# Kernel tuning notes

Hardware: AMD Instinct MI355X
Metric: run time of the kernel (lower is better)

The kernel has to match this reference:

```python
import jax, jax.numpy as jnp
import numpy as np

B, N, E, D = 2, 4096, 1024, 128  # batch, seq, embed_dim, expand_ratio (head dim)
H = E // D                        # 8 heads
LN_EPS = 1e-5


def setup_inputs() -> dict:
    key = jax.random.key(0)
    ks = jax.random.split(key, 6)
    s = 0.02
    return {
        "x": jax.random.normal(ks[0], (B, N, E), jnp.float32),
        "W_in": jax.random.normal(ks[1], (3 * E, E), jnp.float32) * s,
        "W_out": jax.random.normal(ks[2], (E, E), jnp.float32) * s,
        "W_g1": jax.random.normal(ks[3], (D, E), jnp.float32) * s,
        "W_g2": jax.random.normal(ks[4], (E, D), jnp.float32) * s,
        "ln_w": jnp.ones((E,), jnp.float32),
    }


def _gla_scan(q, k, v, g):
    # q,k,v,g: [b,h,n,d]; GLA recurrence: S_t = exp(g_t)[:,None]*S_{t-1} + k_t v_t^T; o_t = q_t @ S_t
    def step(S, inp):
        qt, kt, vt, gt = inp  # each [b,h,d]
        S = jnp.exp(gt)[..., None] * S + kt[..., None] * vt[..., None, :]  # [b,h,d,d]
        ot = jnp.einsum('bhd,bhde->bhe', qt, S)
        return S, ot

    xs = tuple(jnp.moveaxis(a, 2, 0) for a in (q, k, v, g))  # [n,b,h,d]
    S0 = jnp.zeros(q.shape[:2] + (q.shape[-1], v.shape[-1]), q.dtype)
    _, o = jax.lax.scan(step, S0, xs)
    return jnp.moveaxis(o, 0, 2)  # [b,h,n,d]


def reference(x, W_in, W_out, W_g1, W_g2, ln_w):
    b, n, e = x.shape
    u = x @ W_in.T                       # [b,n,3E]
    v, q, lg = jnp.split(u, 3, axis=-1)  # note order: v, q, log_f
    q = jax.nn.silu(q)                   # q_activation = silu
    f = jax.nn.sigmoid(lg)
    k = 1.0 - f                          # non_sparse_ratio == 1 path
    g = jax.nn.log_sigmoid(lg)           # log of forget gate

    def tohead(a):
        return a.reshape(b, n, H, D).transpose(0, 2, 1, 3)  # b h n d

    o = _gla_scan(tohead(q), tohead(k), tohead(v), tohead(g))
    o = o.transpose(0, 2, 1, 3).reshape(b, n, e)  # b n (h d)

    gate = jax.nn.sigmoid((x @ W_g1.T) @ W_g2.T)  # low-rank output gate
    o = o * gate

    mu = jnp.mean(o, axis=-1, keepdims=True)
    var = jnp.var(o, axis=-1, keepdims=True)
    o = (o - mu) * jax.lax.rsqrt(var + LN_EPS) * ln_w  # layernorm, no bias
    return o @ W_out.T
```

## Files before the change

### kernel.cpp

```cpp
#include <hip/hip_runtime.h>
#include <cmath>

#define B_ 2
#define N_ 4096
#define E_ 1024
#define D_ 128
#define H_ 8
#define CHUNK 64
#define NC_ (N_/CHUNK)

__device__ __forceinline__ float sigmoidf_(float x){ return 1.f/(1.f + __expf(-x)); }

__device__ __forceinline__ unsigned short f2bf(float f){
    unsigned u = __float_as_uint(f);
    u += 0x7FFFu + ((u >> 16) & 1u);
    return (unsigned short)(u >> 16);
}
__device__ __forceinline__ float bf2f(unsigned short s){
    return __uint_as_float(((unsigned)s) << 16);
}
__device__ __forceinline__ unsigned short f2bf_fast(float f){
    __bf16 h = (__bf16)f;
    return __builtin_bit_cast(unsigned short, h);
}

typedef __attribute__((ext_vector_type(8))) __bf16 bf16x8;
typedef __attribute__((ext_vector_type(4))) float  f32x4;
typedef __attribute__((address_space(3))) unsigned int as3_u32;
typedef __attribute__((address_space(1))) unsigned int as1_u32;

__device__ __forceinline__ void gload_lds16(const void* g, void* l){
    __builtin_amdgcn_global_load_lds((as1_u32*)g, (as3_u32*)l, 16, 0, 0);
}

__device__ __forceinline__ bf16x8 ldsfrag256(const unsigned short* Lp, int row, int kg){
    return *reinterpret_cast<const bf16x8*>(&Lp[row*128 + ((kg ^ (row&7))<<3)]);
}
__device__ __forceinline__ bf16x8 ldsfrag128(const unsigned short* Lp, int row, int kg){
    return *reinterpret_cast<const bf16x8*>(&Lp[row*64 + ((kg ^ (row&7))<<3)]);
}
__device__ __forceinline__ bf16x8 u4_to_bf(uint4 u){
    return __builtin_bit_cast(bf16x8, u);
}

template<bool OUT_BF16>
__global__ __launch_bounds__(256) void gemm_bf16(
    const unsigned short* __restrict__ A,
    const unsigned short* __restrict__ Bw,
    void* __restrict__ Cout, int M, int N, int K)
{
    __shared__ unsigned short As[128*64];
    __shared__ unsigned short Bs[128*64];
    const int tid  = threadIdx.x;
    const int wave = tid >> 6;
    const int lane = tid & 63;
    const int gx = gridDim.x;
    const int nwg = gx * gridDim.y;
    int bid = blockIdx.y*gx + blockIdx.x;
    bid = (bid & 7)*(nwg >> 3) + (bid >> 3);
    const int m0 = (bid / gx) * 128, n0 = (bid % gx) * 128;
    const int wr = (wave >> 1) * 64;
    const int wc = (wave & 1) * 64;
    const int l15 = lane & 15, l4 = lane >> 4;
    const int p = l15 & 7;

    f32x4 acc[4][4];
#pragma unroll
    for (int i=0;i<4;i++)
#pragma unroll
        for (int j=0;j<4;j++)
#pragma unroll
            for (int q=0;q<4;q++) acc[i][j][q]=0.f;

    const int srow = wave*32 + (lane>>3);
    const int sgrp = lane & 7;

    for (int k0=0; k0<K; k0+=64){
        if (k0) __syncthreads();
#pragma unroll
        for (int i=0;i<4;i++){
            const int r  = srow + 8*i;
            const int cg = sgrp ^ (r & 7);
            gload_lds16(A  + (size_t)(m0 + r)*K + k0 + cg*8, &As[(wave*32 + 8*i)*64]);
            gload_lds16(Bw + (size_t)(n0 + r)*K + k0 + cg*8, &Bs[(wave*32 + 8*i)*64]);
        }
        __syncthreads();
#pragma unroll
        for (int ks=0; ks<2; ks++){
            bf16x8 av[4], bv[4];
            const int tA = (((ks<<2) | l4) ^ p) << 3;
#pragma unroll
            for (int f=0; f<4; f++){
                const int rowA = wr + f*16 + l15;
                const int rowB = wc + f*16 + l15;
                av[f] = *reinterpret_cast<const bf16x8*>(&As[(rowA<<6) + tA]);
                bv[f] = *reinterpret_cast<const bf16x8*>(&Bs[(rowB<<6) + tA]);
            }
#pragma unroll
            for (int fm=0; fm<4; fm++)
#pragma unroll
                for (int fn=0; fn<4; fn++)
                    acc[fm][fn] = __builtin_amdgcn_mfma_f32_16x16x32_bf16(
                        av[fm], bv[fn], acc[fm][fn], 0, 0, 0);
        }
    }
    const int crow0 = m0 + wr + l4*4;
    const int ccol0 = n0 + wc + l15;
    if (!OUT_BF16){
        float* C = (float*)Cout;
#pragma unroll
        for (int fm=0; fm<4; fm++)
#pragma unroll
            for (int fn=0; fn<4; fn++)
#pragma unroll
                for (int j=0;j<4;j++)
                    C[(size_t)(crow0 + fm*16 + j)*N + ccol0 + fn*16] = acc[fm][fn][j];
    } else {
        unsigned short* C = (unsigned short*)Cout;
#pragma unroll
        for (int fm=0; fm<4; fm++)
#pragma unroll
            for (int fn=0; fn<4; fn++)
#pragma unroll
                for (int j=0;j<4;j++)
                    C[(size_t)(crow0 + fm*16 + j)*N + ccol0 + fn*16] = f2bf(acc[fm][fn][j]);
    }
}

#define CQ0 2097152
#define CQ1 786432
#define CQ2 262144
#define CQ3 32768
#define CQ4 32768
__global__ __launch_bounds__(256) void cast_all(
    const float* __restrict__ x,  const float* __restrict__ w1,
    const float* __restrict__ w2, const float* __restrict__ w3,
    const float* __restrict__ w4,
    unsigned short* __restrict__ xb,  unsigned short* __restrict__ w1b,
    unsigned short* __restrict__ w2b, unsigned short* __restrict__ w3b,
    unsigned short* __restrict__ w4b)
{
    const int total = CQ0+CQ1+CQ2+CQ3+CQ4;
    for (int i = blockIdx.x*256 + threadIdx.x; i < total; i += gridDim.x*256){
        const float* src; unsigned short* dst; int off;
        if (i < CQ0){ src=x; dst=xb; off=i; }
        else if (i < CQ0+CQ1){ src=w1; dst=w1b; off=i-CQ0; }
        else if (i < CQ0+CQ1+CQ2){ src=w2; dst=w2b; off=i-CQ0-CQ1; }
        else if (i < CQ0+CQ1+CQ2+CQ3){ src=w3; dst=w3b; off=i-CQ0-CQ1-CQ2; }
        else { src=w4; dst=w4b; off=i-CQ0-CQ1-CQ2-CQ3; }
        const float4 v = reinterpret_cast<const float4*>(src)[off];
        ushort4 o;
        o.x = f2bf(v.x); o.y = f2bf(v.y); o.z = f2bf(v.z); o.w = f2bf(v.w);
        reinterpret_cast<ushort4*>(dst)[off] = o;
    }
}

__global__ __launch_bounds__(512) void gla_prep(
    const unsigned short* __restrict__ u, float* __restrict__ EBC,
    unsigned short* __restrict__ QSb, unsigned short* __restrict__ KINb,
    unsigned short* __restrict__ KINtb, unsigned short* __restrict__ Vtb)
{
    __shared__ float tot[4*128];
    const int bid = blockIdx.x;
    const int c  = bid % NC_;
    const int hh = (bid / NC_) % H_;
    const int b  = bid / (NC_*H_);
    const int d  = threadIdx.x & 127;
    const int qd = threadIdx.x >> 7;
    const int t0 = qd*16;
    const size_t urow0 = ((size_t)b*N_ + (size_t)c*CHUNK)*(3*E_) + (size_t)hh*D_ + d;

    float bl[16], qv[16], vv[16];
#pragma unroll
    for (int i=0;i<16;i++)
        bl[i] = bf2f(u[urow0 + (size_t)(t0+i)*(3*E_) + 2*E_]);
#pragma unroll
    for (int i=0;i<16;i++)
        qv[i] = bf2f(u[urow0 + (size_t)(t0+i)*(3*E_) + E_]);
#pragma unroll
    for (int i=0;i<16;i++)
        vv[i] = bf2f(u[urow0 + (size_t)(t0+i)*(3*E_)]);

    float acc = 0.f;
#pragma unroll
    for (int i=0;i<16;i++){
        const float lg = bl[i];
        const float e  = __expf(-fabsf(lg));
        const float g  = fminf(lg, 0.f) - __logf(1.f + e);
        acc += g;
        bl[i] = acc;
    }
    tot[qd*128 + d] = acc;
    __syncthreads();
    const float s0 = tot[d], s1 = tot[128+d], s2 = tot[256+d], s3 = tot[384+d];
    const float off = (qd>0 ? s0 : 0.f) + (qd>1 ? s1 : 0.f) + (qd>2 ? s2 : 0.f);
    const float bcv = s0 + s1 + s2 + s3;
    const float ebc = __expf(bcv);
    if (threadIdx.x < 128) EBC[(size_t)bid*D_ + d] = ebc;

    unsigned kin_pk[8], v_pk[8];
    float prev = 0.f;
    const size_t obase = (size_t)bid*CHUNK*D_;
#pragma unroll
    for (int i=0;i<16;i++){
        const int t = t0 + i;
        const float Bl = bl[i];
        const float g  = Bl - prev;  prev = Bl;
        const float Bc = Bl + off;
        const float kk = 1.f - __expf(g);
        const float eB = __expf(Bc);
        const float q  = qv[i];
        const float es = __expf(-q);
        const float silu = q * __builtin_amdgcn_rcpf(1.f + es);
        const float qs  = silu * eB;
        const float kin = kk * __builtin_amdgcn_rcpf(eB);
        QSb [obase + (size_t)t*D_ + d] = f2bf_fast(qs);
        KINb[obase + (size_t)t*D_ + d] = f2bf_fast(kin);
        const unsigned kb = f2bf_fast(kin * ebc);
        const unsigned vb = f2bf_fast(vv[i]);
        if (i & 1){ kin_pk[i>>1] |= kb<<16; v_pk[i>>1] |= vb<<16; }
        else      { kin_pk[i>>1]  = kb;     v_pk[i>>1]  = vb;     }
    }
    const size_t tbase = (size_t)bid*D_*CHUNK + (size_t)d*CHUNK + t0;
#pragma unroll
    for (int j=0;j<2;j++){
        uint4 kq, vq;
        kq.x=kin_pk[4*j]; kq.y=kin_pk[4*j+1]; kq.z=kin_pk[4*j+2]; kq.w=kin_pk[4*j+3];
        vq.x=v_pk[4*j];   vq.y=v_pk[4*j+1];   vq.z=v_pk[4*j+2];   vq.w=v_pk[4*j+3];
        *reinterpret_cast<uint4*>(&KINtb[tbase + j*8]) = kq;
        *reinterpret_cast<uint4*>(&Vtb  [tbase + j*8]) = vq;
    }
}

__global__ __launch_bounds__(256) void gla_chunk_mm(
    const unsigned short* __restrict__ Vtb,
    const unsigned short* __restrict__ KINtb,
    unsigned short* __restrict__ McTb)
{
    __shared__ unsigned short As[128*64];
    __shared__ unsigned short Bs[128*64];
    const int bid = blockIdx.x;
    const int tid = threadIdx.x;
    const int w = tid >> 6, lane = tid & 63;
    const int l15 = lane & 15, l4 = lane >> 4;
    const int wr = (w >> 1) * 64, wc = (w & 1) * 64;
    const unsigned short* A  = Vtb   + (size_t)bid*128*64;
    const unsigned short* Bp = KINtb + (size_t)bid*128*64;

    f32x4 acc[4][4];
#pragma unroll
    for (int i=0;i<4;i++)
#pragma unroll
        for (int j=0;j<4;j++)
#pragma unroll
            for (int q=0;q<4;q++) acc[i][j][q]=0.f;

#pragma unroll
    for (int i=0;i<4;i++){
        const int r  = w*32 + i*8 + (lane>>3);
        const int gs = (lane&7) ^ (r&7);
        gload_lds16(A  + (size_t)r*64 + gs*8, &As[(w*32+i*8)*64]);
        gload_lds16(Bp + (size_t)r*64 + gs*8, &Bs[(w*32+i*8)*64]);
    }
    __syncthreads();
#pragma unroll
    for (int ks=0; ks<2; ks++){
        bf16x8 av[4], bv[4];
#pragma unroll
        for (int f=0; f<4; f++){
            av[f] = ldsfrag128(As, wr + f*16 + l15, ks*4 + l4);
            bv[f] = ldsfrag128(Bs, wc + f*16 + l15, ks*4 + l4);
        }
#pragma unroll
        for (int fm=0; fm<4; fm++)
#pragma unroll
            for (int fn=0; fn<4; fn++)
                acc[fm][fn] = __builtin_amdgcn_mfma_f32_16x16x32_bf16(
                    av[fm], bv[fn], acc[fm][fn], 0, 0, 0);
    }
    unsigned short* C = McTb + (size_t)bid*128*128;
#pragma unroll
    for (int fm=0; fm<4; fm++)
#pragma unroll
        for (int fn=0; fn<4; fn++)
#pragma unroll
            for (int j=0;j<4;j++)
                C[(size_t)(wr + fm*16 + l4*4 + j)*128 + wc + fn*16 + l15] = f2bf(acc[fm][fn][j]);
}

__global__ __launch_bounds__(256) void gla_scan_chunks(
    const unsigned short* __restrict__ McTb, const float* __restrict__ EBC,
    unsigned short* __restrict__ Sb16)
{
    const size_t F = (size_t)blockIdx.x*256 + threadIdx.x;
    const int bh = (int)(F >> 14);
    const int rem = (int)(F & 16383);
    const int d = rem & 127;
    float S = 0.f;
    for (int c=0;c<NC_;c++){
        const size_t idx = (((size_t)bh*NC_ + c) << 14) + rem;
        const float m = bf2f(McTb[idx]);
        const float dec = EBC[((size_t)bh*NC_ + c)*D_ + d];
        Sb16[idx] = f2bf(S);
        S = dec*S + m;
    }
}

__global__ __launch_bounds__(256) void gla_output(
    const unsigned short* __restrict__ QSb,
    const unsigned short* __restrict__ KINb,
    const unsigned short* __restrict__ Vtb,
    const unsigned short* __restrict__ Sb,
    const unsigned short* __restrict__ G2b,
    unsigned short* __restrict__ Opre)
{
    __shared__ unsigned short QS_l[64*128];
    __shared__ unsigned short A_l [64*64];
    const int bid = blockIdx.x;
    const int c = bid % NC_;
    const int h = (bid / NC_) % H_;
    const int b = bid / (NC_*H_);
    const int tid = threadIdx.x;
    const int w = tid >> 6, lane = tid & 63;
    const int l15 = lane & 15, l4 = lane >> 4;

    const unsigned short* qb = QSb + (size_t)bid*64*128;
    const unsigned short* kb = KINb + (size_t)bid*64*128;
    const unsigned short* vb = Vtb + (size_t)bid*128*64;
    const unsigned short* sb = Sb  + (size_t)bid*128*128;

#pragma unroll
    for (int i=0;i<4;i++){
        const int r  = w*16 + i*4 + (lane>>4);
        const int gs = (lane&15) ^ (r&7);
        gload_lds16(qb + (size_t)r*128 + gs*8, &QS_l[(w*16+i*4)*128]);
    }
    uint4 kinr[4];
    {
        const int srow = w*16 + l15;
#pragma unroll
        for (int ks=0; ks<4; ks++)
            kinr[ks] = *reinterpret_cast<const uint4*>(kb + (size_t)srow*128 + (ks*4 + l4)*8);
    }
    __syncthreads();

    uint4 vtr[2][2], sr[2][4];
#pragma unroll
    for (int fe=0; fe<2; fe++){
        const int row = w*32 + fe*16 + l15;
#pragma unroll
        for (int ks=0; ks<2; ks++)
            vtr[fe][ks] = *reinterpret_cast<const uint4*>(vb + (size_t)row*64 + (ks*4 + l4)*8);
#pragma unroll
        for (int ks=0; ks<4; ks++)
            sr[fe][ks]  = *reinterpret_cast<const uint4*>(sb + (size_t)row*128 + (ks*4 + l4)*8);
    }

    f32x4 accA[4];
#pragma unroll
    for (int i=0;i<4;i++)
#pragma unroll
        for (int q=0;q<4;q++) accA[i][q]=0.f;
#pragma unroll
    for (int ks=0; ks<4; ks++){
        const bf16x8 bv = u4_to_bf(kinr[ks]);
#pragma unroll
        for (int ft=0; ft<4; ft++){
            const bf16x8 av = ldsfrag256(QS_l, ft*16 + l15, ks*4 + l4);
            accA[ft] = __builtin_amdgcn_mfma_f32_16x16x32_bf16(av, bv, accA[ft], 0,0,0);
        }
    }
#pragma unroll
    for (int ft=0; ft<4; ft++)
#pragma unroll
        for (int j=0;j<4;j++){
            const int t = ft*16 + l4*4 + j;
            const int s = w*16 + l15;
            const float vA = (t >= s) ? accA[ft][j] : 0.f;
            A_l[t*64 + (((s>>3) ^ (t&7))<<3) + (s&7)] = f2bf(vA);
        }
    __syncthreads();

    f32x4 acc[4][2];
#pragma unroll
    for (int i=0;i<4;i++)
#pragma unroll
        for (int j=0;j<2;j++)
#pragma unroll
            for (int q=0;q<4;q++) acc[i][j][q]=0.f;
#pragma unroll
    for (int ks=0; ks<2; ks++){
        const bf16x8 b0 = u4_to_bf(vtr[0][ks]);
        const bf16x8 b1 = u4_to_bf(vtr[1][ks]);
#pragma unroll
        for (int ft=0; ft<4; ft++){
            const bf16x8 av = ldsfrag128(A_l, ft*16 + l15, ks*4 + l4);
            acc[ft][0] = __builtin_amdgcn_mfma_f32_16x16x32_bf16(av, b0, acc[ft][0], 0,0,0);
            acc[ft][1] = __builtin_amdgcn_mfma_f32_16x16x32_bf16(av, b1, acc[ft][1], 0,0,0);
        }
    }
#pragma unroll
    for (int ks=0; ks<4; ks++){
        const bf16x8 b0 = u4_to_bf(sr[0][ks]);
        const bf16x8 b1 = u4_to_bf(sr[1][ks]);
#pragma unroll
        for (int ft=0; ft<4; ft++){
            const bf16x8 av = ldsfrag256(QS_l, ft*16 + l15, ks*4 + l4);
            acc[ft][0] = __builtin_amdgcn_mfma_f32_16x16x32_bf16(av, b0, acc[ft][0], 0,0,0);
            acc[ft][1] = __builtin_amdgcn_mfma_f32_16x16x32_bf16(av, b1, acc[ft][1], 0,0,0);
        }
    }
    const size_t rowbase = (size_t)b*N_ + (size_t)c*CHUNK;
#pragma unroll
    for (int ft=0; ft<4; ft++)
#pragma unroll
        for (int fe=0; fe<2; fe++)
#pragma unroll
            for (int j=0;j<4;j++){
                const int t = ft*16 + l4*4 + j;
                const int e = w*32 + fe*16 + l15;
                const size_t idx = (rowbase + t)*E_ + h*D_ + e;
                const float g = sigmoidf_(bf2f(G2b[idx]));
                Opre[idx] = f2bf(acc[ft][fe][j] * g);
            }
}

__global__ __launch_bounds__(256) void ln_bf16(
    const unsigned short* __restrict__ O, const float* __restrict__ lnw,
    unsigned short* __restrict__ Ob)
{
    const int row = blockIdx.x;
    const int tid = threadIdx.x;
    const size_t off = (size_t)row*E_ + tid*4;
    const ushort4 ov = *reinterpret_cast<const ushort4*>(&O[off]);
    float4 o;
    o.x = bf2f(ov.x); o.y = bf2f(ov.y); o.z = bf2f(ov.z); o.w = bf2f(ov.w);
    float s1 = o.x+o.y+o.z+o.w;
    float s2 = o.x*o.x + o.y*o.y + o.z*o.z + o.w*o.w;
#pragma unroll
    for (int sh=32; sh>0; sh>>=1){
        s1 += __shfl_down(s1, sh);
        s2 += __shfl_down(s2, sh);
    }
    __shared__ float r1[4], r2[4];
    const int wid = tid >> 6;
    if ((tid & 63)==0){ r1[wid]=s1; r2[wid]=s2; }
    __syncthreads();
    s1 = r1[0]+r1[1]+r1[2]+r1[3];
    s2 = r2[0]+r2[1]+r2[2]+r2[3];
    const float mean = s1 * (1.f/E_);
    const float var  = s2 * (1.f/E_) - mean*mean;
    const float rs   = rsqrtf(var + 1e-5f);
    const float4 w = *reinterpret_cast<const float4*>(&lnw[tid*4]);
    ushort4 r;
    r.x = f2bf((o.x-mean)*rs*w.x); r.y = f2bf((o.y-mean)*rs*w.y);
    r.z = f2bf((o.z-mean)*rs*w.z); r.w = f2bf((o.w-mean)*rs*w.w);
    *reinterpret_cast<ushort4*>(&Ob[off]) = r;
}

extern "C" void kernel_launch(void* const* d_in, const int* in_sizes, int n_in,
                              void* d_out, int out_size, void* d_ws, size_t ws_size,
                              hipStream_t stream)
{
    const float* x     = (const float*)d_in[0];
    const float* W_in  = (const float*)d_in[1];
    const float* W_out = (const float*)d_in[2];
    const float* W_g1  = (const float*)d_in[3];
    const float* W_g2  = (const float*)d_in[4];
    const float* lnw   = (const float*)d_in[5];
    float* out = (float*)d_out;
    char* ws = (char*)d_ws;

    unsigned short* ub     = (unsigned short*)(ws);
    unsigned short* McTb   = (unsigned short*)(ws);
    unsigned short* Sb16   = (unsigned short*)(ws + 33554432);
    unsigned short* G2b    = (unsigned short*)(ws + 67108864);
    float*          EBC    = (float*)(ws + 100663296);
    unsigned short* QSb    = (unsigned short*)(ws + 101187584);
    unsigned short* KINb   = (unsigned short*)(ws + 117964800);
    unsigned short* KINtb  = (unsigned short*)(ws + 134742016);
    unsigned short* Vtb    = (unsigned short*)(ws + 151519232);
    unsigned short* Opre   = (unsigned short*)(ws + 168296448);
    unsigned short* xb     = (unsigned short*)(ws + 201850880);
    unsigned short* W_inb  = (unsigned short*)(ws + 218628096);
    unsigned short* W_outb = (unsigned short*)(ws + 224919552);
    unsigned short* W_g1b  = (unsigned short*)(ws + 227016704);
    unsigned short* W_g2b  = (unsigned short*)(ws + 227278848);
    unsigned short* G1b    = (unsigned short*)(ws + 227540992);
    unsigned short* ObF    = (unsigned short*)(ws + 229638144);

    const int M = B_*N_;
    dim3 blk(256);

    cast_all<<<2048, blk, 0, stream>>>(x, W_in, W_out, W_g1, W_g2,
                                       xb, W_inb, W_outb, W_g1b, W_g2b);

    gemm_bf16<true><<<dim3(3*E_/128, M/128), blk, 0, stream>>>(xb, W_inb, ub, M, 3*E_, E_);
    gla_prep<<<dim3(B_*H_*NC_), dim3(512), 0, stream>>>(ub, EBC, QSb, KINb, KINtb, Vtb);
    gla_chunk_mm<<<dim3(B_*H_*NC_), blk, 0, stream>>>(Vtb, KINtb, McTb);
    gla_scan_chunks<<<dim3((B_*H_*D_*D_)/256), blk, 0, stream>>>(McTb, EBC, Sb16);
    gemm_bf16<true><<<dim3(1, M/128), blk, 0, stream>>>(xb, W_g1b, G1b, M, D_, E_);
    gemm_bf16<true><<<dim3(E_/128, M/128), blk, 0, stream>>>(G1b, W_g2b, G2b, M, E_, D_);
    gla_output<<<dim3(B_*H_*NC_), blk, 0, stream>>>(QSb, KINb, Vtb, Sb16, G2b, Opre);
    ln_bf16<<<dim3(M), blk, 0, stream>>>(Opre, lnw, ObF);
    gemm_bf16<false><<<dim3(E_/128, M/128), blk, 0, stream>>>(ObF, W_outb, out, M, E_, E_);
}
```

Measured before the change: 202.7 us.

## Fuse x cast into input GEMM and merge low-rank gate projection

The input GEMM now reads fp32 x directly and converts to bf16 while staging into LDS, removing the separate cast pass over x. W_g1 is concatenated onto W_in so the first gate projection is computed in the same GEMM, and the second gate GEMM reads that slice with a strided lda. This drops a kernel launch and a full write/read of bf16 x, at the cost of a register-path A load instead of direct-to-LDS loads in the largest GEMM.

```diff
diff --git a/kernel.cpp b/kernel.cpp
--- a/kernel.cpp
+++ b/kernel.cpp
@@ -8,6 +8,7 @@
 #define H_ 8
 #define CHUNK 64
 #define NC_ (N_/CHUNK)
+#define UW_ (3*E_ + D_)
 
 __device__ __forceinline__ float sigmoidf_(float x){ return 1.f/(1.f + __expf(-x)); }
 
@@ -43,11 +44,11 @@
     return __builtin_bit_cast(bf16x8, u);
 }
 
-template<bool OUT_BF16>
+template<bool A_F32, bool OUT_BF16>
 __global__ __launch_bounds__(256) void gemm_bf16(
-    const unsigned short* __restrict__ A,
+    const void* __restrict__ A,
     const unsigned short* __restrict__ Bw,
-    void* __restrict__ Cout, int M, int N, int K)
+    void* __restrict__ Cout, int M, int N, int K, int lda)
 {
     __shared__ unsigned short As[128*64];
     __shared__ unsigned short Bs[128*64];
@@ -77,11 +78,35 @@
 
     for (int k0=0; k0<K; k0+=64){
         if (k0) __syncthreads();
+        if constexpr (A_F32){
+            const float* Af = (const float*)A;
+#pragma unroll
+            for (int g=0; g<4; g++){
+                const int slot = g*256 + tid;
+                const int row = slot >> 3, grp = slot & 7;
+                const float* src = Af + (size_t)(m0+row)*lda + k0 + grp*8;
+                const float4 f0 = *reinterpret_cast<const float4*>(src);
+                const float4 f1 = *reinterpret_cast<const float4*>(src + 4);
+                uint4 pk;
+                pk.x = (unsigned)f2bf(f0.x) | ((unsigned)f2bf(f0.y)<<16);
+                pk.y = (unsigned)f2bf(f0.z) | ((unsigned)f2bf(f0.w)<<16);
+                pk.z = (unsigned)f2bf(f1.x) | ((unsigned)f2bf(f1.y)<<16);
+                pk.w = (unsigned)f2bf(f1.z) | ((unsigned)f2bf(f1.w)<<16);
+                *reinterpret_cast<uint4*>(&As[(row<<6) + ((grp ^ (row&7))<<3)]) = pk;
+            }
+        } else {
+            const unsigned short* Ab = (const unsigned short*)A;
+#pragma unroll
+            for (int i=0;i<4;i++){
+                const int r  = srow + 8*i;
+                const int cg = sgrp ^ (r & 7);
+                gload_lds16(Ab + (size_t)(m0 + r)*lda + k0 + cg*8, &As[(wave*32 + 8*i)*64]);
+            }
+        }
 #pragma unroll
         for (int i=0;i<4;i++){
             const int r  = srow + 8*i;
             const int cg = sgrp ^ (r & 7);
-            gload_lds16(A  + (size_t)(m0 + r)*K + k0 + cg*8, &As[(wave*32 + 8*i)*64]);
             gload_lds16(Bw + (size_t)(n0 + r)*K + k0 + cg*8, &Bs[(wave*32 + 8*i)*64]);
         }
         __syncthreads();
@@ -127,27 +152,23 @@
     }
 }
 
-#define CQ0 2097152
-#define CQ1 786432
-#define CQ2 262144
-#define CQ3 32768
-#define CQ4 32768
-__global__ __launch_bounds__(256) void cast_all(
-    const float* __restrict__ x,  const float* __restrict__ w1,
-    const float* __restrict__ w2, const float* __restrict__ w3,
-    const float* __restrict__ w4,
-    unsigned short* __restrict__ xb,  unsigned short* __restrict__ w1b,
-    unsigned short* __restrict__ w2b, unsigned short* __restrict__ w3b,
-    unsigned short* __restrict__ w4b)
-{
-    const int total = CQ0+CQ1+CQ2+CQ3+CQ4;
+#define WQ1 786432
+#define WQ3 32768
+#define WQ2 262144
+#define WQ4 32768
+__global__ __launch_bounds__(256) void cast_w(
+    const float* __restrict__ w1, const float* __restrict__ w3,
+    const float* __restrict__ w2, const float* __restrict__ w4,
+    unsigned short* __restrict__ wcat,
+    unsigned short* __restrict__ w2b, unsigned short* __restrict__ w4b)
+{
+    const int total = WQ1+WQ3+WQ2+WQ4;
     for (int i = blockIdx.x*256 + threadIdx.x; i < total; i += gridDim.x*256){
         const float* src; unsigned short* dst; int off;
-        if (i < CQ0){ src=x; dst=xb; off=i; }
-        else if (i < CQ0+CQ1){ src=w1; dst=w1b; off=i-CQ0; }
-        else if (i < CQ0+CQ1+CQ2){ src=w2; dst=w2b; off=i-CQ0-CQ1; }
-        else if (i < CQ0+CQ1+CQ2+CQ3){ src=w3; dst=w3b; off=i-CQ0-CQ1-CQ2; }
-        else { src=w4; dst=w4b; off=i-CQ0-CQ1-CQ2-CQ3; }
+        if (i < WQ1){ src=w1; dst=wcat; off=i; }
+        else if (i < WQ1+WQ3){ src=w3; dst=wcat+WQ1*4; off=i-WQ1; }
+        else if (i < WQ1+WQ3+WQ2){ src=w2; dst=w2b; off=i-WQ1-WQ3; }
+        else { src=w4; dst=w4b; off=i-WQ1-WQ3-WQ2; }
         const float4 v = reinterpret_cast<const float4*>(src)[off];
         ushort4 o;
         o.x = f2bf(v.x); o.y = f2bf(v.y); o.z = f2bf(v.z); o.w = f2bf(v.w);
@@ -168,18 +189,18 @@
     const int d  = threadIdx.x & 127;
     const int qd = threadIdx.x >> 7;
     const int t0 = qd*16;
-    const size_t urow0 = ((size_t)b*N_ + (size_t)c*CHUNK)*(3*E_) + (size_t)hh*D_ + d;
+    const size_t urow0 = ((size_t)b*N_ + (size_t)c*CHUNK)*UW_ + (size_t)hh*D_ + d;
 
     float bl[16], qv[16], vv[16];
 #pragma unroll
     for (int i=0;i<16;i++)
-        bl[i] = bf2f(u[urow0 + (size_t)(t0+i)*(3*E_) + 2*E_]);
+        bl[i] = bf2f(u[urow0 + (size_t)(t0+i)*UW_ + 2*E_]);
 #pragma unroll
     for (int i=0;i<16;i++)
-        qv[i] = bf2f(u[urow0 + (size_t)(t0+i)*(3*E_) + E_]);
+        qv[i] = bf2f(u[urow0 + (size_t)(t0+i)*UW_ + E_]);
 #pragma unroll
     for (int i=0;i<16;i++)
-        vv[i] = bf2f(u[urow0 + (size_t)(t0+i)*(3*E_)]);
+        vv[i] = bf2f(u[urow0 + (size_t)(t0+i)*UW_]);
 
     float acc = 0.f;
 #pragma unroll
@@ -471,7 +492,7 @@
     float* out = (float*)d_out;
     char* ws = (char*)d_ws;
 
-    unsigned short* ub     = (unsigned short*)(ws);
+    unsigned short* ub2    = (unsigned short*)(ws);
     unsigned short* McTb   = (unsigned short*)(ws);
     unsigned short* Sb16   = (unsigned short*)(ws + 33554432);
     unsigned short* G2b    = (unsigned short*)(ws + 67108864);
@@ -481,27 +502,25 @@
     unsigned short* KINtb  = (unsigned short*)(ws + 134742016);
     unsigned short* Vtb    = (unsigned short*)(ws + 151519232);
     unsigned short* Opre   = (unsigned short*)(ws + 168296448);
-    unsigned short* xb     = (unsigned short*)(ws + 201850880);
-    unsigned short* W_inb  = (unsigned short*)(ws + 218628096);
+    unsigned short* Wcatb  = (unsigned short*)(ws + 201850880);
     unsigned short* W_outb = (unsigned short*)(ws + 224919552);
-    unsigned short* W_g1b  = (unsigned short*)(ws + 227016704);
     unsigned short* W_g2b  = (unsigned short*)(ws + 227278848);
-    unsigned short* G1b    = (unsigned short*)(ws + 227540992);
     unsigned short* ObF    = (unsigned short*)(ws + 229638144);
 
     const int M = B_*N_;
     dim3 blk(256);
 
-    cast_all<<<2048, blk, 0, stream>>>(x, W_in, W_out, W_g1, W_g2,
-                                       xb, W_inb, W_outb, W_g1b, W_g2b);
-
-    gemm_bf16<true><<<dim3(3*E_/128, M/128), blk, 0, stream>>>(xb, W_inb, ub, M, 3*E_, E_);
-    gla_prep<<<dim3(B_*H_*NC_), dim3(512), 0, stream>>>(ub, EBC, QSb, KINb, KINtb, Vtb);
+    cast_w<<<1024, blk, 0, stream>>>(W_in, W_g1, W_out, W_g2, Wcatb, W_outb, W_g2b);
+
+    gemm_bf16<true,true><<<dim3(UW_/128, M/128), blk, 0, stream>>>(
+        x, Wcatb, ub2, M, UW_, E_, E_);
+    gla_prep<<<dim3(B_*H_*NC_), dim3(512), 0, stream>>>(ub2, EBC, QSb, KINb, KINtb, Vtb);
+    gemm_bf16<false,true><<<dim3(E_/128, M/128), blk, 0, stream>>>(
+        ub2 + 3*E_, W_g2b, G2b, M, E_, D_, UW_);
     gla_chunk_mm<<<dim3(B_*H_*NC_), blk, 0, stream>>>(Vtb, KINtb, McTb);
     gla_scan_chunks<<<dim3((B_*H_*D_*D_)/256), blk, 0, stream>>>(McTb, EBC, Sb16);
-    gemm_bf16<true><<<dim3(1, M/128), blk, 0, stream>>>(xb, W_g1b, G1b, M, D_, E_);
-    gemm_bf16<true><<<dim3(E_/128, M/128), blk, 0, stream>>>(G1b, W_g2b, G2b, M, E_, D_);
     gla_output<<<dim3(B_*H_*NC_), blk, 0, stream>>>(QSb, KINb, Vtb, Sb16, G2b, Opre);
     ln_bf16<<<dim3(M), blk, 0, stream>>>(Opre, lnw, ObF);
-    gemm_bf16<false><<<dim3(E_/128, M/128), blk, 0, stream>>>(ObF, W_outb, out, M, E_, E_);
-}
+    gemm_bf16<false,false><<<dim3(E_/128, M/128), blk, 0, stream>>>(
+        ObF, W_outb, out, M, E_, E_, E_);
+}
```

Result: slower. 252.7 us (+24.7%).
